# Performance work log

Hardware: AMD Instinct MI355X
Metric: run time of the kernel (lower is better)

The kernel has to match this reference:

```python
import jax, jax.numpy as jnp
import numpy as np

GAMMA = 2.0
ALPHA = 0.25
NEG_TH = 0.4
POS_TH = 0.5
NUM_CLASSES = 80
STRIDES = [8, 16, 32, 64, 128]
IMG_H, IMG_W = 800, 1024
LEVEL_HW = [(100, 128), (50, 64), (25, 32), (13, 16), (7, 8)]


def _base_anchors(stride):
    # standard RetinaNet: octave_base_scale=4, 3 scales/octave, ratios 0.5/1/2
    scales = 4.0 * stride * np.array([2 ** 0, 2 ** (1.0 / 3), 2 ** (2.0 / 3)])
    ratios = np.array([0.5, 1.0, 2.0])
    h_r = np.sqrt(ratios)
    w_r = 1.0 / h_r
    ws = (w_r[:, None] * scales[None, :]).reshape(-1)
    hs = (h_r[:, None] * scales[None, :]).reshape(-1)
    return np.stack([-ws / 2, -hs / 2, ws / 2, hs / 2], axis=1)  # [9,4]


def build_anchors():
    out = []
    for (h, w), s in zip(LEVEL_HW, STRIDES):
        base = _base_anchors(s)
        xs = (np.arange(w) + 0.5) * s
        ys = (np.arange(h) + 0.5) * s
        cx, cy = np.meshgrid(xs, ys)  # [h,w]
        ctr = np.stack([cx, cy, cx, cy], axis=-1)  # [h,w,4]
        a = ctr[:, :, None, :] + base[None, None, :, :]  # [h,w,9,4] anchor-fastest
        out.append(a.reshape(-1, 4))
    return jnp.asarray(np.concatenate(out, axis=0), dtype=jnp.float32)  # [A,4]


def _iou(gt, an):  # [G,4],[A,4] -> [G,A]
    lt = jnp.maximum(gt[:, None, :2], an[None, :, :2])
    rb = jnp.minimum(gt[:, None, 2:], an[None, :, 2:])
    wh = jnp.clip(rb - lt, 0.0)
    inter = wh[..., 0] * wh[..., 1]
    area_g = (gt[:, 2] - gt[:, 0]) * (gt[:, 3] - gt[:, 1])
    area_a = (an[:, 2] - an[:, 0]) * (an[:, 3] - an[:, 1])
    return inter / (area_g[:, None] + area_a[None, :] - inter + 1e-6)


def _encode(an, gt):  # delta encoding, mean=0 std=1
    aw = an[:, 2] - an[:, 0]
    ah = an[:, 3] - an[:, 1]
    ax = (an[:, 0] + an[:, 2]) * 0.5
    ay = (an[:, 1] + an[:, 3]) * 0.5
    gw = gt[:, 2] - gt[:, 0]
    gh = gt[:, 3] - gt[:, 1]
    gx = (gt[:, 0] + gt[:, 2]) * 0.5
    gy = (gt[:, 1] + gt[:, 3]) * 0.5
    return jnp.stack([(gx - ax) / aw, (gy - ay) / ah, jnp.log(gw / aw), jnp.log(gh / ah)], axis=1)


def _per_image(logits, regp, gtb, gtl, anchors):
    G = gtb.shape[0]
    iou = _iou(gtb, anchors)  # [G,A]
    max_ov = iou.max(axis=0)
    arg_ov = iou.argmax(axis=0)
    assigned = jnp.where(max_ov < NEG_TH, 0, -1)
    assigned = jnp.where(max_ov >= POS_TH, arg_ov + 1, assigned)
    max_gt = iou.max(axis=1)
    eq = iou == max_gt[:, None]
    any_eq = eq.any(axis=0)
    last_j = (G - 1) - jnp.argmax(eq[::-1], axis=0)
    assigned = jnp.where(any_eq, last_j + 1, assigned)
    pos = assigned > 0
    neg = assigned == 0
    gi = jnp.clip(assigned - 1, 0, G - 1)
    labels = jnp.where(pos, gtl[gi], NUM_CLASSES)  # negatives get label = num_classes
    include = (pos | neg).astype(logits.dtype)  # ignored anchors contribute 0
    # focal loss
    p = jnp.clip(jax.nn.sigmoid(logits), 1e-6, 1.0 - 1e-6)
    cr = jnp.arange(NUM_CLASSES)[None, :]
    t = labels[:, None]
    term1 = (1.0 - p) ** GAMMA * jnp.log(p)
    term2 = p ** GAMMA * jnp.log(1.0 - p)
    per = -(t == cr).astype(p.dtype) * term1 * ALPHA - ((t != cr) & (t >= 0)).astype(p.dtype) * term2 * (1.0 - ALPHA)
    cls_sum = (per.sum(axis=1) * include).sum()
    # smooth-free L1 on positives
    reg_t = _encode(anchors, gtb[gi])
    reg_sum = (jnp.abs(regp - reg_t).sum(axis=1) * pos.astype(regp.dtype)).sum()
    return cls_sum, reg_sum, pos.sum()


def _flatten_levels(levels, c):
    n = levels[0].shape[0]
    return jnp.concatenate([p.transpose(0, 2, 3, 1).reshape(n, -1, c) for p in levels], axis=1)


def reference(cls_p0, cls_p1, cls_p2, cls_p3, cls_p4, reg_p0, reg_p1, reg_p2, reg_p3, reg_p4, gt_bboxes, gt_labels):
    anchors = build_anchors()
    cls = _flatten_levels([cls_p0, cls_p1, cls_p2, cls_p3, cls_p4], NUM_CLASSES)  # [N,A,80]
    reg = _flatten_levels([reg_p0, reg_p1, reg_p2, reg_p3, reg_p4], 4)  # [N,A,4]
    cls_s, reg_s, npos = jax.vmap(lambda l, r, b, t: _per_image(l, r, b, t, anchors))(cls, reg, gt_bboxes, gt_labels)
    num_pos = jnp.maximum(npos.sum(), 1).astype(cls.dtype)
    return (cls_s.sum() / num_pos, reg_s.sum() / num_pos)


def setup_inputs() -> dict:
    key = jax.random.key(0)
    ks = jax.random.split(key, 16)
    N, G = 2, 32
    d = {}
    for i, (h, w) in enumerate(LEVEL_HW):
        d[f"cls_p{i}"] = jax.random.normal(ks[i], (N, 9 * NUM_CLASSES, h, w), jnp.float32)
        d[f"reg_p{i}"] = jax.random.normal(ks[5 + i], (N, 9 * 4, h, w), jnp.float32)
    cx = jax.random.uniform(ks[10], (N, G), minval=50.0, maxval=IMG_W - 50.0)
    cy = jax.random.uniform(ks[11], (N, G), minval=50.0, maxval=IMG_H - 50.0)
    bw = jax.random.uniform(ks[12], (N, G), minval=32.0, maxval=300.0)
    bh = jax.random.uniform(ks[13], (N, G), minval=32.0, maxval=300.0)
    x1 = jnp.clip(cx - bw / 2, 0.0, IMG_W - 2.0)
    y1 = jnp.clip(cy - bh / 2, 0.0, IMG_H - 2.0)
    x2 = jnp.clip(cx + bw / 2, x1 + 1.0, float(IMG_W))
    y2 = jnp.clip(cy + bh / 2, y1 + 1.0, float(IMG_H))
    d["gt_bboxes"] = jnp.stack([x1, y1, x2, y2], axis=-1)
    d["gt_labels"] = jax.random.randint(ks[14], (N, G), 0, NUM_CLASSES)
    return d
```

## Files before the change

kernel.cpp:

```cpp
#include <hip/hip_runtime.h>
#include <stdint.h>

namespace {
constexpr int A_TOTAL = 153576;
constexpr int NG      = 32;
constexpr int NIMG    = 2;
constexpr int NCLS    = 80;

constexpr size_t WS_CLS0  = 0;
constexpr size_t WS_REG   = 2048;
constexpr size_t WS_NPOS  = 2056;
constexpr size_t WS_MAXGT = 2112;
constexpr size_t WS_LABEL = 2560;
constexpr size_t WS_ZERO  = 2560;
}

__device__ __attribute__((noinline)) float4 anchor_box(int idx) {
    int base, W, stride;
    if      (idx < 115200) { base = 0;      W = 128; stride = 8;   }
    else if (idx < 144000) { base = 115200; W = 64;  stride = 16;  }
    else if (idx < 151200) { base = 144000; W = 32;  stride = 32;  }
    else if (idx < 153072) { base = 151200; W = 16;  stride = 64;  }
    else                   { base = 153072; W = 8;   stride = 128; }
    int s    = idx - base;
    int cell = s / 9;
    int a    = s - cell * 9;
    int y    = cell / W;
    int x    = cell - y * W;
    int r    = a / 3;
    int k    = a - r * 3;
    double c3 = (k == 0) ? 1.0 : ((k == 1) ? 1.2599210498948731648 : 1.5874010519681994748);
    double hr = (r == 0) ? 0.70710678118654752440 : ((r == 1) ? 1.0 : 1.4142135623730950488);
    double scale = 4.0 * (double)stride * c3;
    double wr  = 1.0 / hr;
    double wsz = wr * scale;
    double hsz = hr * scale;
    double cx  = ((double)x + 0.5) * (double)stride;
    double cy  = ((double)y + 0.5) * (double)stride;
    float4 out;
    out.x = (float)(cx - wsz / 2.0);
    out.y = (float)(cy - hsz / 2.0);
    out.z = (float)(cx + wsz / 2.0);
    out.w = (float)(cy + hsz / 2.0);
    return out;
}

__device__ __attribute__((noinline)) float iou_fn(float4 an, float4 g) {
    float ltx = fmaxf(g.x, an.x), lty = fmaxf(g.y, an.y);
    float rbx = fminf(g.z, an.z), rby = fminf(g.w, an.w);
    float w = fmaxf(rbx - ltx, 0.f), h = fmaxf(rby - lty, 0.f);
    float inter = w * h;
    float ag = (g.z - g.x) * (g.w - g.y);
    float aa = (an.z - an.x) * (an.w - an.y);
    return inter / (ag + aa - inter + 1e-6f);
}

__global__ __launch_bounds__(256)
void kmaxgt(const float* __restrict__ gtb, unsigned* __restrict__ maxgt) {
    int n   = blockIdx.y;
    int tid = threadIdx.x;
    int anchor = blockIdx.x * 256 + tid;
    __shared__ float4   g_s[NG];
    __shared__ unsigned smax[NG];
    if (tid < NG) {
        g_s[tid]  = ((const float4*)gtb)[n * NG + tid];
        smax[tid] = 0u;
    }
    __syncthreads();
    bool  valid = anchor < A_TOTAL;
    float4 an = anchor_box(valid ? anchor : 0);
    int lane = tid & 63;
    for (int j = 0; j < NG; ++j) {
        float iou = valid ? iou_fn(an, g_s[j]) : 0.f;
        for (int off = 32; off; off >>= 1)
            iou = fmaxf(iou, __shfl_xor(iou, off));
        if (lane == 0) atomicMax(&smax[j], __float_as_uint(iou));
    }
    __syncthreads();
    if (tid < NG) atomicMax(&maxgt[n * NG + tid], smax[tid]);
}

__global__ __launch_bounds__(256)
void kassign(const float* __restrict__ gtb, const int* __restrict__ gtl,
             const float* __restrict__ maxgt, uint8_t* __restrict__ labels,
             const float* __restrict__ r0, const float* __restrict__ r1,
             const float* __restrict__ r2, const float* __restrict__ r3,
             const float* __restrict__ r4,
             double* __restrict__ reg_acc, int* __restrict__ npos_acc) {
    int n   = blockIdx.y;
    int tid = threadIdx.x;
    int anchor = blockIdx.x * 256 + tid;
    __shared__ float4 g_s[NG];
    __shared__ float  mg_s[NG];
    __shared__ int    gl_s[NG];
    if (tid < NG) {
        g_s[tid]  = ((const float4*)gtb)[n * NG + tid];
        mg_s[tid] = maxgt[n * NG + tid];
        gl_s[tid] = gtl[n * NG + tid];
    }
    __syncthreads();
    bool  valid = anchor < A_TOTAL;
    float4 an = anchor_box(valid ? anchor : 0);
    float best = -1.f; int arg = 0; int last = -1;
    for (int j = 0; j < NG; ++j) {
        float iou = iou_fn(an, g_s[j]);
        if (iou > best) { best = iou; arg = j; }
        if (iou == mg_s[j]) last = j;
    }
    int assigned = -1;
    if (best < 0.4f)  assigned = 0;
    if (best >= 0.5f) assigned = arg + 1;
    if (last >= 0)    assigned = last + 1;

    float rsum = 0.f; bool pos = false;
    if (valid) {
        int base, HW; const float* rp;
        if      (anchor < 115200) { base = 0;      HW = 12800; rp = r0; }
        else if (anchor < 144000) { base = 115200; HW = 3200;  rp = r1; }
        else if (anchor < 151200) { base = 144000; HW = 800;   rp = r2; }
        else if (anchor < 153072) { base = 151200; HW = 208;   rp = r3; }
        else                      { base = 153072; HW = 56;    rp = r4; }
        int s = anchor - base;
        int cell = s / 9; int a = s - cell * 9;

        uint8_t lab;
        if (assigned > 0) {
            pos = true;
            int gi = assigned - 1;
            lab = (uint8_t)gl_s[gi];
            float aw = an.z - an.x, ah = an.w - an.y;
            float ax = (an.x + an.z) * 0.5f, ay = (an.y + an.w) * 0.5f;
            float4 g = g_s[gi];
            float gw = g.z - g.x, gh = g.w - g.y;
            float gx = (g.x + g.z) * 0.5f, gy = (g.y + g.w) * 0.5f;
            float t0 = (gx - ax) / aw, t1 = (gy - ay) / ah;
            float t2 = __logf(gw / aw), t3 = __logf(gh / ah);
            long off = (long)(n * 36 + a * 4) * HW + cell;
            float p0 = rp[off], p1 = rp[off + HW], p2 = rp[off + 2 * HW], p3 = rp[off + 3 * HW];
            rsum = fabsf(p0 - t0) + fabsf(p1 - t1) + fabsf(p2 - t2) + fabsf(p3 - t3);
        } else {
            lab = (assigned == 0) ? (uint8_t)NCLS : (uint8_t)255;
        }
        labels[n * A_TOTAL + base + a * HW + cell] = lab;
    }
    for (int off = 32; off; off >>= 1) rsum += __shfl_xor(rsum, off);
    unsigned long long bal = __ballot(pos);
    __shared__ float pr[4];
    __shared__ int   pn[4];
    int wid = tid >> 6;
    if ((tid & 63) == 0) { pr[wid] = rsum; pn[wid] = __popcll(bal); }
    __syncthreads();
    if (tid == 0) {
        float s = pr[0] + pr[1] + pr[2] + pr[3];
        int   c = pn[0] + pn[1] + pn[2] + pn[3];
        atomicAdd(reg_acc, (double)s);
        atomicAdd(npos_acc, c);
    }
}

__device__ __forceinline__ float focal(float z, int c, int lab) {
    float e   = __expf(z);
    float u   = 1.f + e;
    float inv = __builtin_amdgcn_rcpf(u);
    float L   = __logf(u);
    float p   = e * inv;
    float t2  = 0.75f * (p * p) * L;
    float t1  = 0.25f * (inv * inv) * (L - z);
    float r   = (c == lab) ? t1 : t2;
    return (lab == 255) ? 0.f : r;
}

template <int HW, int BASE, int BPL>
__device__ float cls_level(const float* __restrict__ cp,
                           const uint8_t* __restrict__ labels, int rel) {
    int slab  = rel / BPL;
    int chunk = rel - slab * BPL;
    int n = slab / 9, a = slab - 9 * n;
    int cell = chunk * 128 + 2 * (int)threadIdx.x;
    if (cell >= HW) return 0.f;
    int lb = n * A_TOTAL + BASE + a * HW + cell;
    int lab0 = labels[lb], lab1 = labels[lb + 1];
    const float* p = cp + (size_t)(n * 720 + a * 80) * HW + cell;
    float acc = 0.f;
#pragma unroll 8
    for (int c = 0; c < NCLS; ++c, p += HW) {
        float2 z = *(const float2*)p;
        acc += focal(z.x, c, lab0);
        acc += focal(z.y, c, lab1);
    }
    return acc;
}

__global__ __launch_bounds__(64)
void kcls(const float* __restrict__ c0, const float* __restrict__ c1,
          const float* __restrict__ c2, const float* __restrict__ c3,
          const float* __restrict__ c4,
          const uint8_t* __restrict__ labels, char* __restrict__ ws) {
    int b = blockIdx.x;
    float v;
    if      (b < 1800) v = cls_level<12800, 0,      100>(c0, labels, b);
    else if (b < 2250) v = cls_level<3200,  115200, 25 >(c1, labels, b - 1800);
    else if (b < 2376) v = cls_level<800,   144000, 7  >(c2, labels, b - 2250);
    else if (b < 2412) v = cls_level<208,   151200, 2  >(c3, labels, b - 2376);
    else               v = cls_level<56,    153072, 1  >(c4, labels, b - 2412);
    for (int off = 32; off; off >>= 1) v += __shfl_xor(v, off);
    if (threadIdx.x == 0)
        atomicAdd((double*)(ws + WS_CLS0 + (size_t)(b & 7) * 256), (double)v);
}

__global__ void kfinal(const char* __restrict__ ws, float* __restrict__ out) {
    double cls = 0.0;
    for (int i = 0; i < 8; ++i) cls += *(const double*)(ws + WS_CLS0 + (size_t)i * 256);
    double reg = *(const double*)(ws + WS_REG);
    int    np  = *(const int*)(ws + WS_NPOS);
    float denom = (float)(np > 1 ? np : 1);
    out[0] = (float)cls / denom;
    out[1] = (float)reg / denom;
}

extern "C" void kernel_launch(void* const* d_in, const int* in_sizes, int n_in,
                              void* d_out, int out_size, void* d_ws, size_t ws_size,
                              hipStream_t stream) {
    static const int HWs[5] = {12800, 3200, 800, 208, 56};
    const float* cls_p[5] = {nullptr, nullptr, nullptr, nullptr, nullptr};
    const float* reg_p[5] = {nullptr, nullptr, nullptr, nullptr, nullptr};
    const float* gtb = nullptr;
    const int*   gtl = nullptr;
    for (int i = 0; i < n_in; ++i) {
        int sz = in_sizes[i];
        if (sz == NIMG * NG * 4) { gtb = (const float*)d_in[i]; continue; }
        if (sz == NIMG * NG)     { gtl = (const int*)d_in[i];   continue; }
        for (int l = 0; l < 5; ++l) {
            if (sz == NIMG * 9 * NCLS * HWs[l]) { cls_p[l] = (const float*)d_in[i]; break; }
            if (sz == NIMG * 9 * 4 * HWs[l])    { reg_p[l] = (const float*)d_in[i]; break; }
        }
    }
    float* out = (float*)d_out;

    char* ws = (char*)d_ws;
    hipMemsetAsync(d_ws, 0, WS_ZERO, stream);
    unsigned* maxgt_u = (unsigned*)(ws + WS_MAXGT);
    float*    maxgt_f = (float*)(ws + WS_MAXGT);
    uint8_t*  labels  = (uint8_t*)(ws + WS_LABEL);
    double*   reg_acc = (double*)(ws + WS_REG);
    int*      npos    = (int*)(ws + WS_NPOS);

    dim3 gAB((A_TOTAL + 255) / 256, NIMG);
    kmaxgt<<<gAB, 256, 0, stream>>>(gtb, maxgt_u);
    kassign<<<gAB, 256, 0, stream>>>(gtb, gtl, maxgt_f, labels,
                                     reg_p[0], reg_p[1], reg_p[2], reg_p[3], reg_p[4],
                                     reg_acc, npos);
    kcls<<<2430, 64, 0, stream>>>(cls_p[0], cls_p[1], cls_p[2], cls_p[3], cls_p[4],
                                  labels, ws);
    kfinal<<<1, 1, 0, stream>>>(ws, out);
}
```

Baseline: 218.3 us.

## Restructure max-IoU, widen cls loads, fuse final reduction into cls kernel

```diff
diff --git a/kernel.cpp b/kernel.cpp
--- a/kernel.cpp
+++ b/kernel.cpp
@@ -10,6 +10,7 @@
 constexpr size_t WS_CLS0  = 0;
 constexpr size_t WS_REG   = 2048;
 constexpr size_t WS_NPOS  = 2056;
+constexpr size_t WS_CNT   = 2064;
 constexpr size_t WS_MAXGT = 2112;
 constexpr size_t WS_LABEL = 2560;
 constexpr size_t WS_ZERO  = 2560;
@@ -59,7 +60,7 @@
 void kmaxgt(const float* __restrict__ gtb, unsigned* __restrict__ maxgt) {
     int n   = blockIdx.y;
     int tid = threadIdx.x;
-    int anchor = blockIdx.x * 256 + tid;
+    __shared__ float4   abox[256];
     __shared__ float4   g_s[NG];
     __shared__ unsigned smax[NG];
     if (tid < NG) {
@@ -67,15 +68,22 @@
         smax[tid] = 0u;
     }
     __syncthreads();
-    bool  valid = anchor < A_TOTAL;
-    float4 an = anchor_box(valid ? anchor : 0);
-    int lane = tid & 63;
-    for (int j = 0; j < NG; ++j) {
-        float iou = valid ? iou_fn(an, g_s[j]) : 0.f;
-        for (int off = 32; off; off >>= 1)
-            iou = fmaxf(iou, __shfl_xor(iou, off));
-        if (lane == 0) atomicMax(&smax[j], __float_as_uint(iou));
-    }
+    int j = tid & 31, grp = tid >> 5;
+    float4 gj = g_s[j];
+    float lmax = 0.f;
+    int a0 = blockIdx.x * 1280;
+    for (int r = 0; r < 5; ++r) {
+        int anchor = a0 + r * 256 + tid;
+        float4 bx = (anchor < A_TOTAL) ? anchor_box(anchor)
+                                       : make_float4(0.f, 0.f, 0.f, 0.f);
+        __syncthreads();
+        abox[tid] = bx;
+        __syncthreads();
+#pragma unroll
+        for (int t = 0; t < 32; ++t)
+            lmax = fmaxf(lmax, iou_fn(abox[grp * 32 + t], gj));
+    }
+    atomicMax(&smax[j], __float_as_uint(lmax));
     __syncthreads();
     if (tid < NG) atomicMax(&maxgt[n * NG + tid], smax[tid]);
 }
@@ -164,58 +172,72 @@
     float inv = __builtin_amdgcn_rcpf(u);
     float L   = __logf(u);
     float p   = e * inv;
-    float t2  = 0.75f * (p * p) * L;
-    float t1  = 0.25f * (inv * inv) * (L - z);
-    float r   = (c == lab) ? t1 : t2;
+    float r   = (c == lab) ? 0.25f * (inv * inv) * (L - z)
+                           : 0.75f * (p * p) * L;
     return (lab == 255) ? 0.f : r;
 }
 
-template <int HW, int BASE, int BPL>
-__device__ float cls_level(const float* __restrict__ cp,
-                           const uint8_t* __restrict__ labels, int rel) {
-    int slab  = rel / BPL;
-    int chunk = rel - slab * BPL;
-    int n = slab / 9, a = slab - 9 * n;
-    int cell = chunk * 128 + 2 * (int)threadIdx.x;
-    if (cell >= HW) return 0.f;
-    int lb = n * A_TOTAL + BASE + a * HW + cell;
-    int lab0 = labels[lb], lab1 = labels[lb + 1];
-    const float* p = cp + (size_t)(n * 720 + a * 80) * HW + cell;
-    float acc = 0.f;
-#pragma unroll 8
-    for (int c = 0; c < NCLS; ++c, p += HW) {
-        float2 z = *(const float2*)p;
-        acc += focal(z.x, c, lab0);
-        acc += focal(z.y, c, lab1);
-    }
-    return acc;
-}
-
-__global__ __launch_bounds__(64)
+__global__ __launch_bounds__(256)
 void kcls(const float* __restrict__ c0, const float* __restrict__ c1,
           const float* __restrict__ c2, const float* __restrict__ c3,
           const float* __restrict__ c4,
-          const uint8_t* __restrict__ labels, char* __restrict__ ws) {
-    int b = blockIdx.x;
-    float v;
-    if      (b < 1800) v = cls_level<12800, 0,      100>(c0, labels, b);
-    else if (b < 2250) v = cls_level<3200,  115200, 25 >(c1, labels, b - 1800);
-    else if (b < 2376) v = cls_level<800,   144000, 7  >(c2, labels, b - 2250);
-    else if (b < 2412) v = cls_level<208,   151200, 2  >(c3, labels, b - 2376);
-    else               v = cls_level<56,    153072, 1  >(c4, labels, b - 2412);
+          const uint8_t* __restrict__ labels, char* __restrict__ ws,
+          float* __restrict__ out) {
+    int w    = blockIdx.x * 4 + ((int)threadIdx.x >> 6);
+    int lane = (int)threadIdx.x & 63;
+    const float* cp; int HW, BASE, CH, rel;
+    if      (w < 1800) { cp = c0; HW = 12800; BASE = 0;      CH = 50; rel = w;        }
+    else if (w < 2268) { cp = c1; HW = 3200;  BASE = 115200; CH = 13; rel = w - 1800; }
+    else if (w < 2412) { cp = c2; HW = 800;   BASE = 144000; CH = 4;  rel = w - 2268; }
+    else if (w < 2448) { cp = c3; HW = 208;   BASE = 151200; CH = 1;  rel = w - 2412; }
+    else               { cp = c4; HW = 56;    BASE = 153072; CH = 1;  rel = w - 2448; }
+    int half  = rel & 1;
+    int task  = rel >> 1;
+    int slab  = task / CH;
+    int chunk = task - slab * CH;
+    int n = slab / 9, a = slab - 9 * n;
+    int cell = chunk * 256 + lane * 4;
+    float v = 0.f;
+    if (cell < HW) {
+        int lb = n * A_TOTAL + BASE + a * HW + cell;
+        uchar4 lab4 = *(const uchar4*)(labels + lb);
+        const float* p = cp + (size_t)(n * 720 + a * 80 + half * 40) * HW + cell;
+        int cbase = half * 40;
+        float acc = 0.f;
+#pragma unroll 8
+        for (int c = 0; c < 40; ++c, p += HW) {
+            float4 z = *(const float4*)p;
+            int cc = cbase + c;
+            acc += focal(z.x, cc, lab4.x);
+            acc += focal(z.y, cc, lab4.y);
+            acc += focal(z.z, cc, lab4.z);
+            acc += focal(z.w, cc, lab4.w);
+        }
+        v = acc;
+    }
     for (int off = 32; off; off >>= 1) v += __shfl_xor(v, off);
-    if (threadIdx.x == 0)
-        atomicAdd((double*)(ws + WS_CLS0 + (size_t)(b & 7) * 256), (double)v);
-}
-
-__global__ void kfinal(const char* __restrict__ ws, float* __restrict__ out) {
-    double cls = 0.0;
-    for (int i = 0; i < 8; ++i) cls += *(const double*)(ws + WS_CLS0 + (size_t)i * 256);
-    double reg = *(const double*)(ws + WS_REG);
-    int    np  = *(const int*)(ws + WS_NPOS);
-    float denom = (float)(np > 1 ? np : 1);
-    out[0] = (float)cls / denom;
-    out[1] = (float)reg / denom;
+    if (lane == 0)
+        atomicAdd((double*)(ws + WS_CLS0 + (size_t)(w & 7) * 256), (double)v);
+
+    __shared__ int amlast;
+    __syncthreads();
+    if (threadIdx.x == 0) {
+        __threadfence();
+        int old = atomicAdd((int*)(ws + WS_CNT), 1);
+        amlast = (old == (int)gridDim.x - 1) ? 1 : 0;
+    }
+    __syncthreads();
+    if (amlast && threadIdx.x == 0) {
+        __threadfence();
+        double cls = 0.0;
+        for (int i = 0; i < 8; ++i)
+            cls += atomicAdd((double*)(ws + WS_CLS0 + (size_t)i * 256), 0.0);
+        double reg = atomicAdd((double*)(ws + WS_REG), 0.0);
+        int    np  = atomicAdd((int*)(ws + WS_NPOS), 0);
+        float denom = (float)(np > 1 ? np : 1);
+        out[0] = (float)cls / denom;
+        out[1] = (float)reg / denom;
+    }
 }
 
 extern "C" void kernel_launch(void* const* d_in, const int* in_sizes, int n_in,
@@ -245,12 +267,10 @@
     double*   reg_acc = (double*)(ws + WS_REG);
     int*      npos    = (int*)(ws + WS_NPOS);
 
-    dim3 gAB((A_TOTAL + 255) / 256, NIMG);
-    kmaxgt<<<gAB, 256, 0, stream>>>(gtb, maxgt_u);
-    kassign<<<gAB, 256, 0, stream>>>(gtb, gtl, maxgt_f, labels,
-                                     reg_p[0], reg_p[1], reg_p[2], reg_p[3], reg_p[4],
-                                     reg_acc, npos);
-    kcls<<<2430, 64, 0, stream>>>(cls_p[0], cls_p[1], cls_p[2], cls_p[3], cls_p[4],
-                                  labels, ws);
-    kfinal<<<1, 1, 0, stream>>>(ws, out);
-}
+    kmaxgt<<<dim3(120, NIMG), 256, 0, stream>>>(gtb, maxgt_u);
+    kassign<<<dim3((A_TOTAL + 255) / 256, NIMG), 256, 0, stream>>>(
+        gtb, gtl, maxgt_f, labels,
+        reg_p[0], reg_p[1], reg_p[2], reg_p[3], reg_p[4], reg_acc, npos);
+    kcls<<<621, 256, 0, stream>>>(cls_p[0], cls_p[1], cls_p[2], cls_p[3], cls_p[4],
+                                  labels, ws, out);
+}
```

New measurement: 242.8 us. +11.2%, slower.
